# Kernel optimization log

Measured on AMD Instinct MI355X. Metric: run time of the kernel, lower is better.

The kernel has to match this reference:

```python
import jax, jax.numpy as jnp
import numpy as np

GAMMA = 0.99
LMBDA = 0.95


def setup_inputs() -> dict:
    key = jax.random.key(0)
    k1, k2, k3, k4 = jax.random.split(key, 4)
    B, T = 4096, 2048
    return {
        "reward": jax.random.normal(k1, (B, T), dtype=jnp.float32),
        "terminated": jax.random.randint(k2, (B, T), 0, 2, dtype=jnp.int32),
        "value": jax.random.normal(k3, (B, T), dtype=jnp.float32),
        "next_value": jax.random.normal(k4, (B, T), dtype=jnp.float32),
    }


def _gae(reward, not_done, value, next_value):
    # All inputs [B, T]. Backward-time scan over T with carry gae [B].
    # delta_t = r_t + gamma * V(s_{t+1}) * nd_t - V(s_t)
    # A_t = delta_t + gamma * lmbda * nd_t * A_{t+1}
    xs = (reward.T, not_done.T, value.T, next_value.T)  # each [T, B]

    def step(gae, x):
        r, nd, v, nv = x
        delta = r + GAMMA * nv * nd - v
        gae = delta + GAMMA * LMBDA * nd * gae
        return gae, gae

    init = jnp.zeros(reward.shape[0], dtype=reward.dtype)
    _, adv_t = jax.lax.scan(step, init, xs, reverse=True)  # [T, B]
    advantages = adv_t.T  # [B, T]
    returns = advantages + value
    return advantages, returns


def reference(reward, terminated, value, next_value):
    not_done = 1.0 - terminated.astype(reward.dtype)
    return _gae(reward, not_done, value, next_value)
```

## Files before the change

### kernel.cpp

```cpp
#include <hip/hip_runtime.h>


constexpr float GAMMA = 0.99f;
constexpr float LMBDA = 0.95f;
constexpr int   T     = 2048;
constexpr int   TPB   = 256;
constexpr int   E     = T / TPB;

__global__ __launch_bounds__(TPB) void gae_kernel(
    const float* __restrict__ reward,
    const int*   __restrict__ term,
    const float* __restrict__ value,
    const float* __restrict__ next_value,
    float* __restrict__ adv_out,
    float* __restrict__ ret_out)
{
    const int b = blockIdx.x;
    const int j = threadIdx.x;
    const size_t base = (size_t)b * T + (size_t)j * E;

    float4 rA = ((const float4*)(reward     + base))[0];
    float4 rB = ((const float4*)(reward     + base))[1];
    int4   tA = ((const int4*  )(term       + base))[0];
    int4   tB = ((const int4*  )(term       + base))[1];
    float4 vA = ((const float4*)(value      + base))[0];
    float4 vB = ((const float4*)(value      + base))[1];
    float4 nA = ((const float4*)(next_value + base))[0];
    float4 nB = ((const float4*)(next_value + base))[1];

    float r [E] = {rA.x, rA.y, rA.z, rA.w, rB.x, rB.y, rB.z, rB.w};
    float nd[E] = {1.f - (float)tA.x, 1.f - (float)tA.y, 1.f - (float)tA.z, 1.f - (float)tA.w,
                   1.f - (float)tB.x, 1.f - (float)tB.y, 1.f - (float)tB.z, 1.f - (float)tB.w};
    float v [E] = {vA.x, vA.y, vA.z, vA.w, vB.x, vB.y, vB.z, vB.w};
    float nv[E] = {nA.x, nA.y, nA.z, nA.w, nB.x, nB.y, nB.z, nB.w};

    float loc[E], P[E];
    float g = 0.f, p = 1.f;
    #pragma unroll
    for (int t = E - 1; t >= 0; --t) {
        float c     = (GAMMA * LMBDA) * nd[t];
        float delta = fmaf(GAMMA * nv[t], nd[t], r[t]) - v[t];
        g = fmaf(c, g, delta);
        p *= c;
        loc[t] = g;
        P[t]   = p;
    }

    __shared__ float sA[TPB], sB[TPB];
    sA[j] = loc[0];
    sB[j] = P[0];
    __syncthreads();
    #pragma unroll
    for (int off = 1; off < TPB; off <<= 1) {
        float a1 = sA[j], b1 = sB[j];
        float a2 = 0.f, b2 = 0.f;
        const int k = j + off;
        const bool valid = (k < TPB);
        if (valid) { a2 = sA[k]; b2 = sB[k]; }
        __syncthreads();
        if (valid) {
            sA[j] = fmaf(b1, a2, a1);
            sB[j] = b1 * b2;
        }
        __syncthreads();
    }
    const float gin = (j + 1 < TPB) ? sA[j + 1] : 0.f;

    float adv[E], ret[E];
    #pragma unroll
    for (int t = 0; t < E; ++t) {
        adv[t] = fmaf(P[t], gin, loc[t]);
        ret[t] = adv[t] + v[t];
    }

    ((float4*)(adv_out + base))[0] = make_float4(adv[0], adv[1], adv[2], adv[3]);
    ((float4*)(adv_out + base))[1] = make_float4(adv[4], adv[5], adv[6], adv[7]);
    ((float4*)(ret_out + base))[0] = make_float4(ret[0], ret[1], ret[2], ret[3]);
    ((float4*)(ret_out + base))[1] = make_float4(ret[4], ret[5], ret[6], ret[7]);
}

extern "C" void kernel_launch(void* const* d_in, const int* in_sizes, int n_in,
                              void* d_out, int out_size, void* d_ws, size_t ws_size,
                              hipStream_t stream) {
    const float* reward     = (const float*)d_in[0];
    const int*   term       = (const int*  )d_in[1];
    const float* value      = (const float*)d_in[2];
    const float* next_value = (const float*)d_in[3];

    const int BT = in_sizes[0];
    const int B  = BT / T;

    float* adv = (float*)d_out;
    float* ret = adv + BT;

    gae_kernel<<<B, TPB, 0, stream>>>(reward, term, value, next_value, adv, ret);
}
```

Measured before the change: 177.9 us.

## Map one row per wavefront and replace shared-memory scan with shuffle scan

Each row of 2048 steps is now handled by one 64-lane wavefront, with 32 elements per lane, and each block packs four rows. The block-wide shared-memory Hillis-Steele scan, which needed barriers, becomes a wave-level __shfl_down scan with no __syncthreads. Advantages are recomputed in a second serial pass seeded by the scanned carry, which replaces the stored per-element products. Per-thread memory accesses now stride 128 bytes apart across lanes, so coalescing is weaker, and holding three 32-element register arrays raises register pressure.

```diff
diff --git a/kernel.cpp b/kernel.cpp
--- a/kernel.cpp
+++ b/kernel.cpp
@@ -4,79 +4,82 @@
 constexpr float GAMMA = 0.99f;
 constexpr float LMBDA = 0.95f;
 constexpr int   T     = 2048;
-constexpr int   TPB   = 256;
-constexpr int   E     = T / TPB;
+constexpr int   EPL   = 32;
+constexpr int   ROWS_PER_BLOCK = 4;
 
-__global__ __launch_bounds__(TPB) void gae_kernel(
+__global__ __launch_bounds__(256, 4) void gae_kernel(
     const float* __restrict__ reward,
     const int*   __restrict__ term,
     const float* __restrict__ value,
     const float* __restrict__ next_value,
     float* __restrict__ adv_out,
-    float* __restrict__ ret_out)
+    float* __restrict__ ret_out,
+    int B)
 {
-    const int b = blockIdx.x;
-    const int j = threadIdx.x;
-    const size_t base = (size_t)b * T + (size_t)j * E;
+    const int wave = threadIdx.x >> 6;
+    const int lane = threadIdx.x & 63;
+    const int row  = blockIdx.x * ROWS_PER_BLOCK + wave;
+    if (row >= B) return;
 
-    float4 rA = ((const float4*)(reward     + base))[0];
-    float4 rB = ((const float4*)(reward     + base))[1];
-    int4   tA = ((const int4*  )(term       + base))[0];
-    int4   tB = ((const int4*  )(term       + base))[1];
-    float4 vA = ((const float4*)(value      + base))[0];
-    float4 vB = ((const float4*)(value      + base))[1];
-    float4 nA = ((const float4*)(next_value + base))[0];
-    float4 nB = ((const float4*)(next_value + base))[1];
+    const size_t base = (size_t)row * T + (size_t)lane * EPL;
+    const float4* r4 = (const float4*)(reward     + base);
+    const int4*   t4 = (const int4*  )(term       + base);
+    const float4* v4 = (const float4*)(value      + base);
+    const float4* n4 = (const float4*)(next_value + base);
 
-    float r [E] = {rA.x, rA.y, rA.z, rA.w, rB.x, rB.y, rB.z, rB.w};
-    float nd[E] = {1.f - (float)tA.x, 1.f - (float)tA.y, 1.f - (float)tA.z, 1.f - (float)tA.w,
-                   1.f - (float)tB.x, 1.f - (float)tB.y, 1.f - (float)tB.z, 1.f - (float)tB.w};
-    float v [E] = {vA.x, vA.y, vA.z, vA.w, vB.x, vB.y, vB.z, vB.w};
-    float nv[E] = {nA.x, nA.y, nA.z, nA.w, nB.x, nB.y, nB.z, nB.w};
-
-    float loc[E], P[E];
-    float g = 0.f, p = 1.f;
+    float c[EPL], delta[EPL], vv[EPL];
     #pragma unroll
-    for (int t = E - 1; t >= 0; --t) {
-        float c     = (GAMMA * LMBDA) * nd[t];
-        float delta = fmaf(GAMMA * nv[t], nd[t], r[t]) - v[t];
-        g = fmaf(c, g, delta);
-        p *= c;
-        loc[t] = g;
-        P[t]   = p;
+    for (int q = 0; q < EPL / 4; ++q) {
+        float4 r  = r4[q];
+        int4   tm = t4[q];
+        float4 v  = v4[q];
+        float4 nv = n4[q];
+        float nd0 = 1.f - (float)tm.x, nd1 = 1.f - (float)tm.y;
+        float nd2 = 1.f - (float)tm.z, nd3 = 1.f - (float)tm.w;
+        c[4*q+0] = (GAMMA * LMBDA) * nd0;
+        c[4*q+1] = (GAMMA * LMBDA) * nd1;
+        c[4*q+2] = (GAMMA * LMBDA) * nd2;
+        c[4*q+3] = (GAMMA * LMBDA) * nd3;
+        delta[4*q+0] = fmaf(GAMMA * nv.x, nd0, r.x) - v.x;
+        delta[4*q+1] = fmaf(GAMMA * nv.y, nd1, r.y) - v.y;
+        delta[4*q+2] = fmaf(GAMMA * nv.z, nd2, r.z) - v.z;
+        delta[4*q+3] = fmaf(GAMMA * nv.w, nd3, r.w) - v.w;
+        vv[4*q+0] = v.x; vv[4*q+1] = v.y; vv[4*q+2] = v.z; vv[4*q+3] = v.w;
     }
 
-    __shared__ float sA[TPB], sB[TPB];
-    sA[j] = loc[0];
-    sB[j] = P[0];
-    __syncthreads();
+    float A = 0.f, Bc = 1.f;
     #pragma unroll
-    for (int off = 1; off < TPB; off <<= 1) {
-        float a1 = sA[j], b1 = sB[j];
-        float a2 = 0.f, b2 = 0.f;
-        const int k = j + off;
-        const bool valid = (k < TPB);
-        if (valid) { a2 = sA[k]; b2 = sB[k]; }
-        __syncthreads();
-        if (valid) {
-            sA[j] = fmaf(b1, a2, a1);
-            sB[j] = b1 * b2;
-        }
-        __syncthreads();
-    }
-    const float gin = (j + 1 < TPB) ? sA[j + 1] : 0.f;
-
-    float adv[E], ret[E];
-    #pragma unroll
-    for (int t = 0; t < E; ++t) {
-        adv[t] = fmaf(P[t], gin, loc[t]);
-        ret[t] = adv[t] + v[t];
+    for (int t = EPL - 1; t >= 0; --t) {
+        A  = fmaf(c[t], A, delta[t]);
+        Bc *= c[t];
     }
 
-    ((float4*)(adv_out + base))[0] = make_float4(adv[0], adv[1], adv[2], adv[3]);
-    ((float4*)(adv_out + base))[1] = make_float4(adv[4], adv[5], adv[6], adv[7]);
-    ((float4*)(ret_out + base))[0] = make_float4(ret[0], ret[1], ret[2], ret[3]);
-    ((float4*)(ret_out + base))[1] = make_float4(ret[4], ret[5], ret[6], ret[7]);
+    #pragma unroll
+    for (int off = 1; off < 64; off <<= 1) {
+        float a2 = __shfl_down(A,  off, 64);
+        float b2 = __shfl_down(Bc, off, 64);
+        if (lane + off < 64) {
+            A  = fmaf(Bc, a2, A);
+            Bc *= b2;
+        }
+    }
+    float gin = __shfl_down(A, 1, 64);
+    if (lane == 63) gin = 0.f;
+
+    float4* advp = (float4*)(adv_out + base);
+    float4* retp = (float4*)(ret_out + base);
+    float g = gin;
+    #pragma unroll
+    for (int q = EPL / 4 - 1; q >= 0; --q) {
+        float a3, a2, a1, a0;
+        g = fmaf(c[4*q+3], g, delta[4*q+3]); a3 = g;
+        g = fmaf(c[4*q+2], g, delta[4*q+2]); a2 = g;
+        g = fmaf(c[4*q+1], g, delta[4*q+1]); a1 = g;
+        g = fmaf(c[4*q+0], g, delta[4*q+0]); a0 = g;
+        advp[q] = make_float4(a0, a1, a2, a3);
+        retp[q] = make_float4(a0 + vv[4*q+0], a1 + vv[4*q+1],
+                              a2 + vv[4*q+2], a3 + vv[4*q+3]);
+    }
 }
 
 extern "C" void kernel_launch(void* const* d_in, const int* in_sizes, int n_in,
@@ -93,5 +96,7 @@
     float* adv = (float*)d_out;
     float* ret = adv + BT;
 
-    gae_kernel<<<B, TPB, 0, stream>>>(reward, term, value, next_value, adv, ret);
+    const int grid = (B + ROWS_PER_BLOCK - 1) / ROWS_PER_BLOCK;
+    gae_kernel<<<grid, 64 * ROWS_PER_BLOCK, 0, stream>>>(
+        reward, term, value, next_value, adv, ret, B);
 }
```

After: 198.8 us. 1.12x slower.
